# Kernel tuning notes

Measured on AMD Instinct MI355X. Metric: run time of the kernel, lower is better.

The kernel has to match this reference:

```python
import jax, jax.numpy as jnp
import numpy as np

WIDTH = 1024
NUM_HEADS = 16
HEAD_DIM = WIDTH // NUM_HEADS  # 64
WINDOW = 256
BATCH = 2
SEQ = 2048
_MIN_LOGITS_VALUE = -1e30


def setup_inputs() -> dict:
    key = jax.random.key(0)
    ks = jax.random.split(key, 6)
    std = 1.0 / np.sqrt(WIDTH)
    x = jax.random.normal(ks[0], (BATCH, SEQ, WIDTH), dtype=jnp.float32)
    Wq = jax.random.normal(ks[1], (WIDTH, WIDTH), dtype=jnp.float32) * std
    Wk = jax.random.normal(ks[2], (HEAD_DIM, WIDTH), dtype=jnp.float32) * std
    Wv = jax.random.normal(ks[3], (HEAD_DIM, WIDTH), dtype=jnp.float32) * std
    Wf = jax.random.normal(ks[4], (WIDTH, WIDTH), dtype=jnp.float32) * std  # variance_scale=1.0
    bf = jnp.zeros((WIDTH,), dtype=jnp.float32)
    return {"x": x, "Wq": Wq, "Wk": Wk, "Wv": Wv, "Wf": Wf, "bf": bf}


def reference(x, Wq, Wk, Wv, Wf, bf):
    b, t, _ = x.shape
    # projections (torch Linear: y = x @ W.T)
    q = (x @ Wq.T).reshape(b, t, NUM_HEADS, HEAD_DIM)  # b t n h
    k = x @ Wk.T  # b t h  (MQA: single shared key head)
    v = x @ Wv.T  # b t h
    scale = 1.0 / np.sqrt(HEAD_DIM)
    # logits: queries per-head against the shared key head
    logits = jnp.einsum('btnh,bsh->bnts', q, k) * scale  # b n t s
    # symmetric local window mask |i - j| <= WINDOW
    pos = jnp.arange(t)
    mask = jnp.abs(pos[:, None] - pos[None, :]) <= WINDOW  # t s
    masked = jnp.where(mask[None, None, :, :], logits, _MIN_LOGITS_VALUE)
    probs = jax.nn.softmax(masked.astype(jnp.float32), axis=-1).astype(logits.dtype)
    out = jnp.einsum('bnts,bsh->btnh', probs, v).reshape(b, t, WIDTH)
    return out @ Wf.T + bf
```

## Files before the change

kernel.cpp:

```cpp
#include <hip/hip_runtime.h>

typedef __bf16 bf16;
typedef __bf16 bf16x8 __attribute__((ext_vector_type(8)));
typedef float  f32x4  __attribute__((ext_vector_type(4)));

#define MFMA(a, b, c) __builtin_amdgcn_mfma_f32_16x16x32_bf16((a), (b), (c), 0, 0, 0)

static constexpr int B_   = 2;
static constexpr int T_   = 2048;
static constexpr int D_   = 1024;
static constexpr int NH_  = 16;
static constexpr int HD_  = 64;
static constexpr int WIN_ = 256;
static constexpr int M_   = B_ * T_;
static constexpr int NQKV = D_ + 2 * HD_;

__device__ __forceinline__ void gld_lds16(const bf16* g, bf16* l) {
  __builtin_amdgcn_global_load_lds(
      (const __attribute__((address_space(1))) void*)g,
      (__attribute__((address_space(3))) void*)l, 16, 0, 0);
}

__global__ __launch_bounds__(256) void conv_all(
    const float* __restrict__ x,  const float* __restrict__ wq,
    const float* __restrict__ wk, const float* __restrict__ wv,
    const float* __restrict__ wf, const float* __restrict__ bv,
    bf16* __restrict__ xc, bf16* __restrict__ wqkv,
    bf16* __restrict__ wfc, bf16* __restrict__ bfc) {
  const long i = (long)(blockIdx.x * 256 + threadIdx.x) * 4;
  const float* src; bf16* dst; long off;
  if      (i < 4194304L) { src = x;  dst = xc;              off = 0; }
  else if (i < 5242880L) { src = wq; dst = wqkv;            off = 4194304L; }
  else if (i < 5308416L) { src = wk; dst = wqkv + 1048576L; off = 5242880L; }
  else if (i < 5373952L) { src = wv; dst = wqkv + 1114112L; off = 5308416L; }
  else if (i < 6422528L) { src = wf; dst = wfc;             off = 5373952L; }
  else if (i < 6423552L) { src = bv; dst = bfc;             off = 6422528L; }
  else return;
  const long j = i - off;
  const float4 v = *(const float4*)(src + j);
  bf16 o[4] = {(bf16)v.x, (bf16)v.y, (bf16)v.z, (bf16)v.w};
  *(uint2*)(dst + j) = *(const uint2*)o;
}

template <int EPI>
__global__ __launch_bounds__(256) void gemm128(
    const bf16* __restrict__ A, const bf16* __restrict__ Bw,
    void* __restrict__ Cout, const bf16* __restrict__ bias,
    bf16* __restrict__ kb, bf16* __restrict__ vT, int N, int K) {
  __shared__ __align__(16) bf16 As[128 * 64];
  __shared__ __align__(16) bf16 Bs[128 * 64];

  const int tid  = threadIdx.x;
  const int w    = tid >> 6;
  const int lane = tid & 63;
  const int quad = lane >> 4;
  const int l16  = lane & 15;
  const int wm   = w & 1;
  const int wn   = w >> 1;
  const int m0   = blockIdx.x * 128;
  const int n0   = blockIdx.y * 128;
  const int lrow = lane >> 3;
  const int lcol = (lane & 7) * 8;

  f32x4 acc[4][4] = {};

  for (int k0 = 0; k0 < K; k0 += 64) {
    __syncthreads();
#pragma unroll
    for (int t = 0; t < 4; ++t) {
      const int inst = w * 4 + t;
      gld_lds16(&A[(size_t)(m0 + inst * 8 + lrow) * K + k0 + lcol],
                &As[inst * 512]);
      gld_lds16(&Bw[(size_t)(n0 + inst * 8 + lrow) * K + k0 + lcol],
                &Bs[inst * 512]);
    }
    __syncthreads();
#pragma unroll
    for (int kk = 0; kk < 64; kk += 32) {
      bf16x8 a[4], b[4];
#pragma unroll
      for (int i = 0; i < 4; ++i)
        a[i] = *(const bf16x8*)&As[(wm * 64 + i * 16 + l16) * 64 + kk + quad * 8];
#pragma unroll
      for (int j = 0; j < 4; ++j)
        b[j] = *(const bf16x8*)&Bs[(wn * 64 + j * 16 + l16) * 64 + kk + quad * 8];
#pragma unroll
      for (int i = 0; i < 4; ++i)
#pragma unroll
        for (int j = 0; j < 4; ++j) acc[i][j] = MFMA(a[i], b[j], acc[i][j]);
    }
  }

#pragma unroll
  for (int i = 0; i < 4; ++i) {
#pragma unroll
    for (int j = 0; j < 4; ++j) {
      const int col     = n0 + wn * 64 + j * 16 + l16;
      const int rowbase = m0 + wm * 64 + i * 16 + quad * 4;
      if (EPI == 1) {
        if (col < D_) {
          bf16* qb = (bf16*)Cout;
#pragma unroll
          for (int r = 0; r < 4; ++r)
            qb[(size_t)(rowbase + r) * D_ + col] = (bf16)acc[i][j][r];
        } else if (col < D_ + HD_) {
#pragma unroll
          for (int r = 0; r < 4; ++r)
            kb[(size_t)(rowbase + r) * HD_ + (col - D_)] = (bf16)acc[i][j][r];
        } else {
          bf16 o[4] = {(bf16)acc[i][j][0], (bf16)acc[i][j][1],
                       (bf16)acc[i][j][2], (bf16)acc[i][j][3]};
          *(uint2*)&vT[(size_t)(col - D_ - HD_) * M_ + rowbase] = *(const uint2*)o;
        }
      } else {
        float* outp = (float*)Cout;
        const float bvv = (float)bias[col];
#pragma unroll
        for (int r = 0; r < 4; ++r)
          outp[(size_t)(rowbase + r) * D_ + col] = acc[i][j][r] + bvv;
      }
    }
  }
}

__global__ __launch_bounds__(256) void attn_win64(
    const bf16* __restrict__ q, const bf16* __restrict__ k,
    const bf16* __restrict__ vT, bf16* __restrict__ o) {
  __shared__ __align__(16) bf16 Qs[64 * 64];
  __shared__ __align__(16) bf16 Ks[64 * 64];
  __shared__ __align__(16) bf16 Vt[64 * 64];
  __shared__ __align__(16) bf16 Ps[64 * 72];

  const int tid  = threadIdx.x;
  const int w    = tid >> 6;
  const int lane = tid & 63;
  const int quad = lane >> 4;
  const int l16  = lane & 15;

  const int t0 = blockIdx.x * 64;
  const int n  = blockIdx.y;
  const int b  = blockIdx.z;
  const float scale = 0.125f;

#pragma unroll
  for (int i = 0; i < 2; ++i) {
    const int row = (tid >> 3) + i * 32;
    const int col = (tid & 7) * 8;
    *(uint4*)(&Qs[row * 64 + col]) =
        *(const uint4*)(&q[((size_t)(b * T_ + t0 + row)) * D_ + n * HD_ + col]);
  }

  f32x4 o_acc[4] = {};
  float l_r[4] = {0.0f, 0.0f, 0.0f, 0.0f};

  for (int st = t0 - WIN_; st <= t0 + WIN_; st += 64) {
    if (st < 0 || st >= T_) continue;

    __syncthreads();
#pragma unroll
    for (int i = 0; i < 2; ++i) {
      const int row = (tid >> 3) + i * 32;
      const int col = (tid & 7) * 8;
      *(uint4*)(&Ks[row * 64 + col]) =
          *(const uint4*)(&k[((size_t)(b * T_ + st + row)) * HD_ + col]);
      *(uint4*)(&Vt[row * 64 + col]) =
          *(const uint4*)(&vT[(size_t)row * M_ + b * T_ + st + col]);
    }
    __syncthreads();

    f32x4 sacc[4] = {};
#pragma unroll
    for (int kk = 0; kk < 64; kk += 32) {
      bf16x8 aq = *(const bf16x8*)(&Qs[(w * 16 + l16) * 64 + kk + quad * 8]);
#pragma unroll
      for (int nt = 0; nt < 4; ++nt) {
        bf16x8 bk = *(const bf16x8*)(&Ks[(nt * 16 + l16) * 64 + kk + quad * 8]);
        sacc[nt] = MFMA(aq, bk, sacc[nt]);
      }
    }

#pragma unroll
    for (int r = 0; r < 4; ++r) {
      const int t = t0 + w * 16 + quad * 4 + r;
#pragma unroll
      for (int nt = 0; nt < 4; ++nt) {
        const int s = st + nt * 16 + l16;
        const int d = t - s;
        float sv = fminf(sacc[nt][r] * scale, 30.0f);
        float p = (d > WIN_ || d < -WIN_) ? 0.0f : __expf(sv);
        l_r[r] += p;
        Ps[(w * 16 + quad * 4 + r) * 72 + nt * 16 + l16] = (bf16)p;
      }
    }
    __syncthreads();

#pragma unroll
    for (int kk = 0; kk < 64; kk += 32) {
      bf16x8 ap = *(const bf16x8*)(&Ps[(w * 16 + l16) * 72 + kk + quad * 8]);
#pragma unroll
      for (int nt = 0; nt < 4; ++nt) {
        bf16x8 bv = *(const bf16x8*)(&Vt[(nt * 16 + l16) * 64 + kk + quad * 8]);
        o_acc[nt] = MFMA(ap, bv, o_acc[nt]);
      }
    }
  }

#pragma unroll
  for (int r = 0; r < 4; ++r) {
#pragma unroll
    for (int off = 1; off < 16; off <<= 1) l_r[r] += __shfl_xor(l_r[r], off);
  }

#pragma unroll
  for (int nt = 0; nt < 4; ++nt) {
#pragma unroll
    for (int r = 0; r < 4; ++r) {
      const int t = t0 + w * 16 + quad * 4 + r;
      const int h = nt * 16 + l16;
      o[((size_t)(b * T_ + t)) * D_ + n * HD_ + h] =
          (bf16)(o_acc[nt][r] / (l_r[r] + 1e-30f));
    }
  }
}

extern "C" void kernel_launch(void* const* d_in, const int* in_sizes, int n_in,
                              void* d_out, int out_size, void* d_ws, size_t ws_size,
                              hipStream_t stream) {
  float* out = (float*)d_out;

  bf16* xc   = (bf16*)d_ws;
  bf16* wqkv = xc   + (size_t)M_ * D_;
  bf16* wfc  = wqkv + (size_t)NQKV * D_;
  bf16* bfc  = wfc  + (size_t)D_ * D_;
  bf16* qb   = bfc  + D_;
  bf16* kb   = qb   + (size_t)M_ * D_;
  bf16* vT   = kb   + (size_t)M_ * HD_;

  dim3 blk(256);
  conv_all<<<dim3((6423552 / 4 + 255) / 256), blk, 0, stream>>>(
      (const float*)d_in[0], (const float*)d_in[1], (const float*)d_in[2],
      (const float*)d_in[3], (const float*)d_in[4], (const float*)d_in[5],
      xc, wqkv, wfc, bfc);

  gemm128<1><<<dim3(M_ / 128, NQKV / 128), blk, 0, stream>>>(
      xc, wqkv, (void*)qb, nullptr, kb, vT, NQKV, D_);

  attn_win64<<<dim3(T_ / 64, NH_, B_), blk, 0, stream>>>(qb, kb, vT, qb);

  gemm128<2><<<dim3(M_ / 128, D_ / 128), blk, 0, stream>>>(
      qb, wfc, (void*)out, bfc, nullptr, nullptr, D_, D_);
}
```

Baseline: 166.1 us.

## Shrink GEMM M-tile to 64 and widen attention query tile to 128

Both GEMMs now use 64x128 tiles instead of 128x128, giving twice as many blocks to fill the many CUs of the device, at the cost of less operand reuse per block. The attention kernel processes 128 query rows per block, with each wave handling two 16-row groups, so every K/V tile loaded into LDS is reused across twice as many queries. The attention kernel also stages Q, K and V with direct global-to-LDS loads. The trade-off is one extra key tile per block, since the widened window covers more positions that are fully masked, and higher register and LDS use per block.

New measurement: 159.5 us. 4.0% less time.

```diff
diff --git a/kernel.cpp b/kernel.cpp
--- a/kernel.cpp
+++ b/kernel.cpp
@@ -43,11 +43,11 @@
 }
 
 template <int EPI>
-__global__ __launch_bounds__(256) void gemm128(
+__global__ __launch_bounds__(256) void gemm64x128(
     const bf16* __restrict__ A, const bf16* __restrict__ Bw,
     void* __restrict__ Cout, const bf16* __restrict__ bias,
     bf16* __restrict__ kb, bf16* __restrict__ vT, int N, int K) {
-  __shared__ __align__(16) bf16 As[128 * 64];
+  __shared__ __align__(16) bf16 As[64 * 64];
   __shared__ __align__(16) bf16 Bs[128 * 64];
 
   const int tid  = threadIdx.x;
@@ -57,46 +57,50 @@
   const int l16  = lane & 15;
   const int wm   = w & 1;
   const int wn   = w >> 1;
-  const int m0   = blockIdx.x * 128;
+  const int m0   = blockIdx.x * 64;
   const int n0   = blockIdx.y * 128;
   const int lrow = lane >> 3;
   const int lcol = (lane & 7) * 8;
 
-  f32x4 acc[4][4] = {};
+  f32x4 acc[2][4] = {};
 
   for (int k0 = 0; k0 < K; k0 += 64) {
     __syncthreads();
 #pragma unroll
-    for (int t = 0; t < 4; ++t) {
-      const int inst = w * 4 + t;
-      gld_lds16(&A[(size_t)(m0 + inst * 8 + lrow) * K + k0 + lcol],
-                &As[inst * 512]);
-      gld_lds16(&Bw[(size_t)(n0 + inst * 8 + lrow) * K + k0 + lcol],
-                &Bs[inst * 512]);
+    for (int t = 0; t < 6; ++t) {
+      const int inst = w * 6 + t;
+      if (inst < 8) {
+        gld_lds16(&A[(size_t)(m0 + inst * 8 + lrow) * K + k0 + lcol],
+                  &As[inst * 512]);
+      } else {
+        const int bi = inst - 8;
+        gld_lds16(&Bw[(size_t)(n0 + bi * 8 + lrow) * K + k0 + lcol],
+                  &Bs[bi * 512]);
+      }
     }
     __syncthreads();
 #pragma unroll
     for (int kk = 0; kk < 64; kk += 32) {
-      bf16x8 a[4], b[4];
-#pragma unroll
-      for (int i = 0; i < 4; ++i)
-        a[i] = *(const bf16x8*)&As[(wm * 64 + i * 16 + l16) * 64 + kk + quad * 8];
+      bf16x8 a[2], b[4];
+#pragma unroll
+      for (int i = 0; i < 2; ++i)
+        a[i] = *(const bf16x8*)&As[(wm * 32 + i * 16 + l16) * 64 + kk + quad * 8];
 #pragma unroll
       for (int j = 0; j < 4; ++j)
         b[j] = *(const bf16x8*)&Bs[(wn * 64 + j * 16 + l16) * 64 + kk + quad * 8];
 #pragma unroll
-      for (int i = 0; i < 4; ++i)
+      for (int i = 0; i < 2; ++i)
 #pragma unroll
         for (int j = 0; j < 4; ++j) acc[i][j] = MFMA(a[i], b[j], acc[i][j]);
     }
   }
 
 #pragma unroll
-  for (int i = 0; i < 4; ++i) {
+  for (int i = 0; i < 2; ++i) {
 #pragma unroll
     for (int j = 0; j < 4; ++j) {
       const int col     = n0 + wn * 64 + j * 16 + l16;
-      const int rowbase = m0 + wm * 64 + i * 16 + quad * 4;
+      const int rowbase = m0 + wm * 32 + i * 16 + quad * 4;
       if (EPI == 1) {
         if (col < D_) {
           bf16* qb = (bf16*)Cout;
@@ -123,102 +127,119 @@
   }
 }
 
-__global__ __launch_bounds__(256) void attn_win64(
+__global__ __launch_bounds__(256) void attn_win128(
     const bf16* __restrict__ q, const bf16* __restrict__ k,
     const bf16* __restrict__ vT, bf16* __restrict__ o) {
-  __shared__ __align__(16) bf16 Qs[64 * 64];
+  __shared__ __align__(16) bf16 Qs[128 * 64];
   __shared__ __align__(16) bf16 Ks[64 * 64];
   __shared__ __align__(16) bf16 Vt[64 * 64];
-  __shared__ __align__(16) bf16 Ps[64 * 72];
+  __shared__ __align__(16) bf16 Ps[128 * 72];
 
   const int tid  = threadIdx.x;
   const int w    = tid >> 6;
   const int lane = tid & 63;
   const int quad = lane >> 4;
   const int l16  = lane & 15;
-
-  const int t0 = blockIdx.x * 64;
+  const int lrow = lane >> 3;
+  const int lcol = (lane & 7) * 8;
+
+  const int t0 = blockIdx.x * 128;
   const int n  = blockIdx.y;
   const int b  = blockIdx.z;
   const float scale = 0.125f;
 
 #pragma unroll
-  for (int i = 0; i < 2; ++i) {
-    const int row = (tid >> 3) + i * 32;
-    const int col = (tid & 7) * 8;
-    *(uint4*)(&Qs[row * 64 + col]) =
-        *(const uint4*)(&q[((size_t)(b * T_ + t0 + row)) * D_ + n * HD_ + col]);
-  }
-
-  f32x4 o_acc[4] = {};
-  float l_r[4] = {0.0f, 0.0f, 0.0f, 0.0f};
-
-  for (int st = t0 - WIN_; st <= t0 + WIN_; st += 64) {
+  for (int t = 0; t < 4; ++t) {
+    const int inst = w * 4 + t;
+    gld_lds16(&q[((size_t)(b * T_ + t0 + inst * 8 + lrow)) * D_ + n * HD_ + lcol],
+              &Qs[inst * 512]);
+  }
+
+  f32x4 o_acc[2][4] = {};
+  float l_r[2][4] = {};
+
+  for (int st = t0 - WIN_; st <= t0 + WIN_ + 64; st += 64) {
     if (st < 0 || st >= T_) continue;
 
     __syncthreads();
 #pragma unroll
-    for (int i = 0; i < 2; ++i) {
-      const int row = (tid >> 3) + i * 32;
-      const int col = (tid & 7) * 8;
-      *(uint4*)(&Ks[row * 64 + col]) =
-          *(const uint4*)(&k[((size_t)(b * T_ + st + row)) * HD_ + col]);
-      *(uint4*)(&Vt[row * 64 + col]) =
-          *(const uint4*)(&vT[(size_t)row * M_ + b * T_ + st + col]);
-    }
-    __syncthreads();
-
-    f32x4 sacc[4] = {};
+    for (int t = 0; t < 2; ++t) {
+      const int inst = w * 2 + t;
+      gld_lds16(&k[((size_t)(b * T_ + st + inst * 8 + lrow)) * HD_ + lcol],
+                &Ks[inst * 512]);
+      gld_lds16(&vT[(size_t)(inst * 8 + lrow) * M_ + b * T_ + st + lcol],
+                &Vt[inst * 512]);
+    }
+    __syncthreads();
+
+    f32x4 sacc[2][4] = {};
 #pragma unroll
     for (int kk = 0; kk < 64; kk += 32) {
-      bf16x8 aq = *(const bf16x8*)(&Qs[(w * 16 + l16) * 64 + kk + quad * 8]);
+      bf16x8 aq[2];
+#pragma unroll
+      for (int rg = 0; rg < 2; ++rg)
+        aq[rg] = *(const bf16x8*)&Qs[(w * 32 + rg * 16 + l16) * 64 + kk + quad * 8];
 #pragma unroll
       for (int nt = 0; nt < 4; ++nt) {
-        bf16x8 bk = *(const bf16x8*)(&Ks[(nt * 16 + l16) * 64 + kk + quad * 8]);
-        sacc[nt] = MFMA(aq, bk, sacc[nt]);
-      }
-    }
-
-#pragma unroll
-    for (int r = 0; r < 4; ++r) {
-      const int t = t0 + w * 16 + quad * 4 + r;
+        bf16x8 bk = *(const bf16x8*)&Ks[(nt * 16 + l16) * 64 + kk + quad * 8];
+#pragma unroll
+        for (int rg = 0; rg < 2; ++rg) sacc[rg][nt] = MFMA(aq[rg], bk, sacc[rg][nt]);
+      }
+    }
+
+#pragma unroll
+    for (int rg = 0; rg < 2; ++rg) {
+#pragma unroll
+      for (int r = 0; r < 4; ++r) {
+        const int t = t0 + w * 32 + rg * 16 + quad * 4 + r;
+#pragma unroll
+        for (int nt = 0; nt < 4; ++nt) {
+          const int s = st + nt * 16 + l16;
+          const int d = t - s;
+          float sv = fminf(sacc[rg][nt][r] * scale, 30.0f);
+          float p = (d > WIN_ || d < -WIN_) ? 0.0f : __expf(sv);
+          l_r[rg][r] += p;
+          Ps[(w * 32 + rg * 16 + quad * 4 + r) * 72 + nt * 16 + l16] = (bf16)p;
+        }
+      }
+    }
+    __syncthreads();
+
+#pragma unroll
+    for (int kk = 0; kk < 64; kk += 32) {
+      bf16x8 ap[2];
+#pragma unroll
+      for (int rg = 0; rg < 2; ++rg)
+        ap[rg] = *(const bf16x8*)&Ps[(w * 32 + rg * 16 + l16) * 72 + kk + quad * 8];
 #pragma unroll
       for (int nt = 0; nt < 4; ++nt) {
-        const int s = st + nt * 16 + l16;
-        const int d = t - s;
-        float sv = fminf(sacc[nt][r] * scale, 30.0f);
-        float p = (d > WIN_ || d < -WIN_) ? 0.0f : __expf(sv);
-        l_r[r] += p;
-        Ps[(w * 16 + quad * 4 + r) * 72 + nt * 16 + l16] = (bf16)p;
-      }
-    }
-    __syncthreads();
-
-#pragma unroll
-    for (int kk = 0; kk < 64; kk += 32) {
-      bf16x8 ap = *(const bf16x8*)(&Ps[(w * 16 + l16) * 72 + kk + quad * 8]);
-#pragma unroll
-      for (int nt = 0; nt < 4; ++nt) {
-        bf16x8 bv = *(const bf16x8*)(&Vt[(nt * 16 + l16) * 64 + kk + quad * 8]);
-        o_acc[nt] = MFMA(ap, bv, o_acc[nt]);
-      }
-    }
-  }
-
-#pragma unroll
-  for (int r = 0; r < 4; ++r) {
-#pragma unroll
-    for (int off = 1; off < 16; off <<= 1) l_r[r] += __shfl_xor(l_r[r], off);
-  }
-
-#pragma unroll
-  for (int nt = 0; nt < 4; ++nt) {
-#pragma unroll
-    for (int r = 0; r < 4; ++r) {
-      const int t = t0 + w * 16 + quad * 4 + r;
-      const int h = nt * 16 + l16;
-      o[((size_t)(b * T_ + t)) * D_ + n * HD_ + h] =
-          (bf16)(o_acc[nt][r] / (l_r[r] + 1e-30f));
+        bf16x8 bv = *(const bf16x8*)&Vt[(nt * 16 + l16) * 64 + kk + quad * 8];
+#pragma unroll
+        for (int rg = 0; rg < 2; ++rg)
+          o_acc[rg][nt] = MFMA(ap[rg], bv, o_acc[rg][nt]);
+      }
+    }
+  }
+
+#pragma unroll
+  for (int rg = 0; rg < 2; ++rg)
+#pragma unroll
+    for (int r = 0; r < 4; ++r)
+#pragma unroll
+      for (int off = 1; off < 16; off <<= 1)
+        l_r[rg][r] += __shfl_xor(l_r[rg][r], off);
+
+#pragma unroll
+  for (int rg = 0; rg < 2; ++rg) {
+#pragma unroll
+    for (int nt = 0; nt < 4; ++nt) {
+#pragma unroll
+      for (int r = 0; r < 4; ++r) {
+        const int t = t0 + w * 32 + rg * 16 + quad * 4 + r;
+        const int h = nt * 16 + l16;
+        o[((size_t)(b * T_ + t)) * D_ + n * HD_ + h] =
+            (bf16)(o_acc[rg][nt][r] / (l_r[rg][r] + 1e-30f));
+      }
     }
   }
 }
@@ -242,11 +263,11 @@
       (const float*)d_in[3], (const float*)d_in[4], (const float*)d_in[5],
       xc, wqkv, wfc, bfc);
 
-  gemm128<1><<<dim3(M_ / 128, NQKV / 128), blk, 0, stream>>>(
+  gemm64x128<1><<<dim3(M_ / 64, NQKV / 128), blk, 0, stream>>>(
       xc, wqkv, (void*)qb, nullptr, kb, vT, NQKV, D_);
 
-  attn_win64<<<dim3(T_ / 64, NH_, B_), blk, 0, stream>>>(qb, kb, vT, qb);
-
-  gemm128<2><<<dim3(M_ / 128, D_ / 128), blk, 0, stream>>>(
+  attn_win128<<<dim3(T_ / 128, NH_, B_), blk, 0, stream>>>(qb, kb, vT, qb);
+
+  gemm64x128<2><<<dim3(M_ / 64, D_ / 128), blk, 0, stream>>>(
       qb, wfc, (void*)out, bfc, nullptr, nullptr, D_, D_);
 }
```
